# Kernel optimization log

Hardware: AMD Instinct MI355X
Metric: run time of the kernel (lower is better)

The kernel has to match this reference:

```python
import jax, jax.numpy as jnp
import numpy as np

DECAY = 0.99
EPS = 1e-05
LOSS_FACTOR = 0.1


def setup_inputs() -> dict:
    key = jax.random.key(0)
    k1, k2, k3, k4 = jax.random.split(key, 4)
    x = jax.random.normal(k1, (64, 256, 32, 32), dtype=jnp.float32)
    centroids = jax.random.normal(k2, (256, 1024), dtype=jnp.float32)
    cluster_size = jax.random.uniform(k3, (1024,), dtype=jnp.float32)
    centroids_avg = jax.random.normal(k4, (256, 1024), dtype=jnp.float32)
    return {"x": x, "centroids": centroids, "cluster_size": cluster_size,
            "centroids_avg": centroids_avg}


def _forward(x, centroids, cluster_size, centroids_avg):
    F, K = centroids.shape
    # torch: x_flat = x.transpose(-1, 1).contiguous().view(-1, n_features)
    xs = jnp.swapaxes(x, 1, -1)              # [B, W, H, C]
    flat_shape = xs.shape
    xf = xs.reshape(-1, F)                   # [N, F]
    dist = ((xf * xf).sum(1, keepdims=True)
            + (centroids * centroids).sum(0, keepdims=True)
            - 2.0 * (xf @ centroids))        # [N, K]
    ind = jnp.argmin(dist, axis=1)           # [N] nearest centroid
    # training-path EMA updates (one-hot matmuls expressed as segment sums)
    counts = jax.ops.segment_sum(jnp.ones(ind.shape, dtype=xf.dtype), ind,
                                 num_segments=K)              # [K]
    centroids_sum = jax.ops.segment_sum(xf, ind, num_segments=K).T  # [F, K]
    new_cs = DECAY * cluster_size + (1.0 - DECAY) * counts
    new_avg = DECAY * centroids_avg + (1.0 - DECAY) * centroids_sum
    n = new_cs.sum()
    cs_norm = (new_cs + EPS) / (n + K * EPS) * n
    new_centroids = new_avg / cs_norm[None, :]               # [F, K]
    # quantize with updated codebook (embedding lookup)
    xq = new_centroids.T[ind].reshape(flat_shape)            # [B, W, H, C]
    xq = jnp.swapaxes(xq, 1, -1)                             # [B, C, H, W]
    xq_st = x + jax.lax.stop_gradient(xq - x)                # straight-through
    return xq_st, xq


def reference(x, centroids, cluster_size, centroids_avg):
    out, _ = _forward(x, centroids, cluster_size, centroids_avg)
    return out
```

## Files before the change

### kernel.cpp

```cpp
#include <hip/hip_runtime.h>


#define DECAY 0.99f
#define EPSF 1e-5f
#define DELTA 0.05f

typedef _Float16 f16x8 __attribute__((ext_vector_type(8)));
typedef float f32x4 __attribute__((ext_vector_type(4)));

static __device__ __forceinline__ unsigned short h_bits(_Float16 h) {
  return __builtin_bit_cast(unsigned short, h);
}
static __device__ __forceinline__ float h_val(unsigned short u) {
  return (float)__builtin_bit_cast(_Float16, u);
}

__global__ void csq_kernel(const float* __restrict__ cent, float* __restrict__ csq) {
  int k0 = blockIdx.x * 64;
  int t = threadIdx.x;
  int kk = t & 63, cg = t >> 6;
  float s = 0.f;
  for (int c = cg; c < 256; c += 4) {
    float v = cent[(size_t)c * 1024 + k0 + kk];
    s += v * v;
  }
  __shared__ float red[4][64];
  red[cg][kk] = s;
  __syncthreads();
  if (t < 64) csq[k0 + t] = red[0][t] + red[1][t] + red[2][t] + red[3][t];
}

__global__ void centT_kernel(const float* __restrict__ cent, _Float16* __restrict__ ctp) {
  __shared__ float tl[32][33];
  int f0 = (blockIdx.x >> 5) * 32, k0 = (blockIdx.x & 31) * 32;
  int t = threadIdx.x;
#pragma unroll
  for (int i = 0; i < 4; ++i) {
    int fi = (t >> 5) + i * 8, ki = t & 31;
    tl[fi][ki] = cent[(size_t)(f0 + fi) * 1024 + k0 + ki];
  }
  __syncthreads();
#pragma unroll
  for (int i = 0; i < 4; ++i) {
    int ki = (t >> 5) + i * 8, fi = t & 31;
    int k = k0 + ki, f = f0 + fi;
    _Float16 h = (_Float16)tl[fi][ki];
    size_t idx = (size_t)(k >> 4) * 4096 + (size_t)(f >> 5) * 512 +
                 (size_t)(k & 15) * 32 + (size_t)((f >> 3) & 3) * 8 + (f & 7);
    ctp[idx] = h;
  }
}

__global__ void transpose_kernel(const float* __restrict__ x, _Float16* __restrict__ xh,
                                 _Float16* __restrict__ xl) {
  __shared__ float tile[64][65];
  int bid = blockIdx.x;
  int pt = bid & 15, ct = (bid >> 4) & 3, b = bid >> 6;
  int c0 = ct * 64, p0 = pt * 64;
  int t = threadIdx.x;
#pragma unroll
  for (int i = 0; i < 16; ++i) {
    int idx = t + i * 256;
    int ci = idx >> 6, pi = idx & 63;
    tile[ci][pi] = x[((size_t)(b * 256 + c0 + ci) << 10) + p0 + pi];
  }
  __syncthreads();
#pragma unroll
  for (int i = 0; i < 8; ++i) {
    int idx = t + i * 256;
    int pi = idx >> 5, cp = idx & 31;
    int p = p0 + pi;
    int r = ((p & 31) << 5) | (p >> 5);
    float v0 = tile[cp * 2][pi], v1 = tile[cp * 2 + 1][pi];
    _Float16 h0 = (_Float16)v0, h1 = (_Float16)v1;
    _Float16 l0 = (_Float16)(v0 - (float)h0), l1 = (_Float16)(v1 - (float)h1);
    unsigned int uh = (unsigned int)h_bits(h0) | ((unsigned int)h_bits(h1) << 16);
    unsigned int ul = (unsigned int)h_bits(l0) | ((unsigned int)h_bits(l1) << 16);
    size_t base = ((size_t)((b << 10) + r)) * 128 + ct * 32 + cp;
    ((unsigned int*)xh)[base] = uh;
    ((unsigned int*)xl)[base] = ul;
  }
}

__global__ __launch_bounds__(256, 3) void mfma_argmin_kernel(
    const _Float16* __restrict__ xh, const _Float16* __restrict__ ctp,
    const float* __restrict__ csq, int* __restrict__ ind,
    int* __restrict__ flaglist, unsigned int* __restrict__ flagcnt,
    unsigned int* __restrict__ counts) {
  __shared__ _Float16 Ah[64 * 256];
  __shared__ float csql[1024];
  __shared__ float red1[4][64], red2[4][64];
  __shared__ int redk[4][64];
  const int t = threadIdx.x;
  const int lane = t & 63, w = t >> 6;
  const int lr = lane & 15, lg = lane >> 4;
  const int n0 = blockIdx.x * 64;

#pragma unroll
  for (int i = 0; i < 4; ++i) csql[t + i * 256] = csq[t + i * 256];
#pragma unroll
  for (int i = 0; i < 8; ++i) {
    int idx = t + i * 256;
    int row = idx >> 5, c16 = (idx & 31) * 16;
    int sw = c16 ^ ((row & 7) << 4);
    *(f16x8*)((char*)Ah + row * 512 + sw) =
        *(const f16x8*)((const char*)xh + (size_t)(n0 + row) * 512 + c16);
  }
  __syncthreads();

  float b1[4][4], b2v[4][4];
  int bk[4][4];
#pragma unroll
  for (int rt = 0; rt < 4; ++rt)
#pragma unroll
    for (int rg = 0; rg < 4; ++rg) { b1[rt][rg] = 3.4e38f; b2v[rt][rg] = 3.4e38f; bk[rt][rg] = 0; }

  const int swz = (lr & 7) << 4;
  const int boff = (lr * 4 + lg) * 16;
#pragma unroll 1
  for (int ch = 0; ch < 4; ++ch) {
    const int ccb = w * 256 + ch * 64;
    const size_t cbase = (size_t)(ccb >> 4) * 8192 + boff;
    f32x4 acc[4][4];
#pragma unroll
    for (int ct = 0; ct < 4; ++ct)
#pragma unroll
      for (int rt = 0; rt < 4; ++rt) acc[ct][rt] = (f32x4){0.f, 0.f, 0.f, 0.f};

#pragma unroll 1
    for (int ks = 0; ks < 8; ++ks) {
      f16x8 bh[4], ah[4];
#pragma unroll
      for (int ct = 0; ct < 4; ++ct)
        bh[ct] = *(const f16x8*)((const char*)ctp + cbase + (size_t)ct * 8192 + ks * 1024);
#pragma unroll
      for (int rt = 0; rt < 4; ++rt)
        ah[rt] = *(const f16x8*)((const char*)Ah + (rt * 16 + lr) * 512 + ((ks * 64 + lg * 16) ^ swz));
#pragma unroll
      for (int ct = 0; ct < 4; ++ct)
#pragma unroll
        for (int rt = 0; rt < 4; ++rt)
          acc[ct][rt] = __builtin_amdgcn_mfma_f32_16x16x32_f16(ah[rt], bh[ct], acc[ct][rt], 0, 0, 0);
    }
#pragma unroll
    for (int ct = 0; ct < 4; ++ct) {
      const int col = ccb + ct * 16 + lr;
      const float cq = csql[col];
#pragma unroll
      for (int rt = 0; rt < 4; ++rt)
#pragma unroll
        for (int rg = 0; rg < 4; ++rg) {
          float d = cq - 2.f * acc[ct][rt][rg];
          if (d < b1[rt][rg]) {
            b2v[rt][rg] = b1[rt][rg];
            b1[rt][rg] = d;
            bk[rt][rg] = col;
          } else if (d < b2v[rt][rg]) {
            b2v[rt][rg] = d;
          }
        }
    }
  }

#pragma unroll
  for (int rt = 0; rt < 4; ++rt)
#pragma unroll
    for (int rg = 0; rg < 4; ++rg) {
      float v1 = b1[rt][rg], v2 = b2v[rt][rg];
      int kk = bk[rt][rg];
#pragma unroll
      for (int off = 8; off >= 1; off >>= 1) {
        float o1 = __shfl_xor(v1, off);
        int ok = __shfl_xor(kk, off);
        float o2 = __shfl_xor(v2, off);
        float nb2 = fminf(fmaxf(v1, o1), fminf(v2, o2));
        if (o1 < v1 || (o1 == v1 && ok < kk)) { v1 = o1; kk = ok; }
        v2 = nb2;
      }
      if (lr == 0) {
        int row = rt * 16 + lg * 4 + rg;
        red1[w][row] = v1;
        redk[w][row] = kk;
        red2[w][row] = v2;
      }
    }
  __syncthreads();
  if (t < 64) {
    float v1 = red1[0][t], v2 = red2[0][t];
    int kk = redk[0][t];
#pragma unroll
    for (int wi = 1; wi < 4; ++wi) {
      float o1 = red1[wi][t], o2 = red2[wi][t];
      int ok = redk[wi][t];
      float nb2 = fminf(fmaxf(v1, o1), fminf(v2, o2));
      if (o1 < v1 || (o1 == v1 && ok < kk)) { v1 = o1; kk = ok; }
      v2 = nb2;
    }
    ind[n0 + t] = kk;
    atomicAdd(&counts[kk], 1u);
    if (v2 - v1 < DELTA) {
      unsigned int p = atomicAdd(flagcnt, 1u);
      flaglist[p] = n0 + t;
    }
  }
}

__global__ __launch_bounds__(256) void fixup_kernel(
    const _Float16* __restrict__ xh, const _Float16* __restrict__ xl,
    const float* __restrict__ cent, const float* __restrict__ csq,
    const int* __restrict__ flaglist, const unsigned int* __restrict__ flagcnt,
    int* __restrict__ ind, unsigned int* __restrict__ counts) {
  const int t = threadIdx.x;
  const int nf = (int)*flagcnt;
  __shared__ float xrow[256];
  __shared__ float rv[256];
  __shared__ int rk[256];
  for (int ii = blockIdx.x; ii < nf; ii += gridDim.x) {
    __syncthreads();
    int row = flaglist[ii];
    xrow[t] = (float)xh[(size_t)row * 256 + t] + (float)xl[(size_t)row * 256 + t];
    __syncthreads();
    float a0 = 0.f, a1 = 0.f, a2 = 0.f, a3 = 0.f;
#pragma unroll 8
    for (int f = 0; f < 256; ++f) {
      float xs = xrow[f];
      const float* cr = cent + (size_t)f * 1024 + t;
      a0 += xs * cr[0];
      a1 += xs * cr[256];
      a2 += xs * cr[512];
      a3 += xs * cr[768];
    }
    float bd = csq[t] - 2.f * a0;
    int bkk = t;
    float d1 = csq[t + 256] - 2.f * a1;
    if (d1 < bd) { bd = d1; bkk = t + 256; }
    float d2 = csq[t + 512] - 2.f * a2;
    if (d2 < bd) { bd = d2; bkk = t + 512; }
    float d3 = csq[t + 768] - 2.f * a3;
    if (d3 < bd) { bd = d3; bkk = t + 768; }
    rv[t] = bd;
    rk[t] = bkk;
    __syncthreads();
    for (int off = 128; off >= 1; off >>= 1) {
      if (t < off) {
        float ov = rv[t + off];
        int ok = rk[t + off];
        if (ov < rv[t] || (ov == rv[t] && ok < rk[t])) { rv[t] = ov; rk[t] = ok; }
      }
      __syncthreads();
    }
    if (t == 0) {
      int newk = rk[0];
      int oldk = ind[row];
      if (newk != oldk) {
        ind[row] = newk;
        atomicAdd(&counts[oldk], 0xFFFFFFFFu);
        atomicAdd(&counts[newk], 1u);
      }
    }
  }
}

__global__ __launch_bounds__(64) void csnorm_scan_kernel(
    const float* __restrict__ cs, const unsigned int* __restrict__ counts,
    float* __restrict__ icn, unsigned int* __restrict__ offsets,
    unsigned int* __restrict__ cursor) {
  const int t = threadIdx.x;
  unsigned int cl[16];
  float csl[16];
  unsigned int s = 0;
  float css = 0.f;
#pragma unroll
  for (int j = 0; j < 16; ++j) {
    cl[j] = counts[t * 16 + j];
    s += cl[j];
    csl[j] = cs[t * 16 + j];
    css += csl[j];
  }
  unsigned int incl = s;
#pragma unroll
  for (int off = 1; off < 64; off <<= 1) {
    unsigned int v = __shfl_up(incl, off);
    if (t >= off) incl += v;
  }
  unsigned int run = incl - s;
  float tot = css;
#pragma unroll
  for (int off = 32; off >= 1; off >>= 1) tot += __shfl_xor(tot, off);
  const float n = DECAY * tot + (1.f - DECAY) * 65536.f;
#pragma unroll
  for (int j = 0; j < 16; ++j) {
    int k = t * 16 + j;
    offsets[k] = run;
    cursor[k] = run;
    float ncs = DECAY * csl[j] + (1.f - DECAY) * (float)cl[j];
    float csn = (ncs + EPSF) / (n + 1024.f * EPSF) * n;
    icn[k] = 1.f / csn;
    run += cl[j];
  }
  if (t == 63) offsets[1024] = run;
}

__global__ void scatter_kernel(const int* __restrict__ ind, unsigned int* __restrict__ cursor,
                               int* __restrict__ rowlist) {
  int n = blockIdx.x * 256 + threadIdx.x;
  int k = ind[n];
  unsigned int pos = atomicAdd(&cursor[k], 1u);
  rowlist[pos] = n;
}

__global__ __launch_bounds__(256) void sumflush_kernel(
    const _Float16* __restrict__ xh, const int* __restrict__ rowlist,
    const int* __restrict__ ind, float* __restrict__ sums) {
  __shared__ int rl[64];
  __shared__ int kl[64];
  const int t = threadIdx.x;
  const int sub = t >> 6, lane = t & 63;
  const int p0 = blockIdx.x * 64;
  if (t < 64) {
    int r = rowlist[p0 + t];
    rl[t] = r;
    kl[t] = ind[r];
  }
  __syncthreads();
  float a0 = 0.f, a1 = 0.f, a2 = 0.f, a3 = 0.f;
  int curk = kl[sub * 16];
#pragma unroll
  for (int i = 0; i < 16; ++i) {
    int p = sub * 16 + i;
    int k = kl[p];
    if (k != curk) {
      float* dst = &sums[(size_t)curk * 256 + lane * 4];
      atomicAdd(&dst[0], a0);
      atomicAdd(&dst[1], a1);
      atomicAdd(&dst[2], a2);
      atomicAdd(&dst[3], a3);
      a0 = a1 = a2 = a3 = 0.f;
      curk = k;
    }
    int r = rl[p];
    uint2 vh = *(const uint2*)&((const unsigned int*)xh)[(size_t)r * 128 + lane * 2];
    a0 += h_val((unsigned short)(vh.x & 0xFFFF));
    a1 += h_val((unsigned short)(vh.x >> 16));
    a2 += h_val((unsigned short)(vh.y & 0xFFFF));
    a3 += h_val((unsigned short)(vh.y >> 16));
  }
  float* dst = &sums[(size_t)curk * 256 + lane * 4];
  atomicAdd(&dst[0], a0);
  atomicAdd(&dst[1], a1);
  atomicAdd(&dst[2], a2);
  atomicAdd(&dst[3], a3);
}

__global__ __launch_bounds__(256) void newcentT_kernel(
    const float* __restrict__ sums, const float* __restrict__ avg,
    const float* __restrict__ icn, float* __restrict__ nc) {
  __shared__ float tl[32][33];
  const int t = threadIdx.x;
  const int k0 = (blockIdx.x & 31) * 32, f0 = (blockIdx.x >> 5) * 32;
#pragma unroll
  for (int i = 0; i < 4; ++i) {
    int ki = (t >> 5) + i * 8, fi = t & 31;
    tl[ki][fi] = sums[(size_t)(k0 + ki) * 256 + f0 + fi];
  }
  __syncthreads();
#pragma unroll
  for (int i = 0; i < 4; ++i) {
    int fi = (t >> 5) + i * 8, ki = t & 31;
    size_t idx = (size_t)(f0 + fi) * 1024 + k0 + ki;
    nc[idx] = (DECAY * avg[idx] + (1.f - DECAY) * tl[ki][fi]) * icn[k0 + ki];
  }
}

__global__ void gather_kernel(const float* __restrict__ nc, const int* __restrict__ ind,
                              float* __restrict__ out) {
  __shared__ int ip[1024];
  int b = blockIdx.x >> 3;
  int cg = (blockIdx.x & 7) * 32;
  int t = threadIdx.x;
#pragma unroll
  for (int j = 0; j < 4; ++j) {
    int p = t + j * 256;
    int r = ((p & 31) << 5) | (p >> 5);
    ip[p] = ind[(b << 10) + r];
  }
  __syncthreads();
  for (int c = cg; c < cg + 32; ++c) {
    const float* row = nc + (size_t)c * 1024;
#pragma unroll
    for (int j = 0; j < 4; ++j) {
      int p = t + j * 256;
      out[((size_t)(b * 256 + c) << 10) + p] = row[ip[p]];
    }
  }
}

extern "C" void kernel_launch(void* const* d_in, const int* in_sizes, int n_in,
                              void* d_out, int out_size, void* d_ws, size_t ws_size,
                              hipStream_t stream) {
  const float* x = (const float*)d_in[0];
  const float* cent = (const float*)d_in[1];
  const float* cs = (const float*)d_in[2];
  const float* avg = (const float*)d_in[3];
  float* out = (float*)d_out;

  char* ws = (char*)d_ws;
  _Float16* xh = (_Float16*)ws;
  _Float16* xl = (_Float16*)(ws + 33554432);
  _Float16* ctp = (_Float16*)(ws + 67108864);
  float* nc = (float*)(ws + 67108864);
  unsigned int* counts = (unsigned int*)(ws + 68157440);
  unsigned int* flagcnt = (unsigned int*)(ws + 68161536);
  float* csq = (float*)(ws + 68165632);
  float* icn = (float*)(ws + 68169728);
  unsigned int* offsets = (unsigned int*)(ws + 68173824);
  unsigned int* cursor = (unsigned int*)(ws + 68182016);
  int* ind = (int*)(ws + 68186112);
  int* flaglist = (int*)(ws + 68448256);
  int* rowlist = (int*)(ws + 68448256);
  float* sums = (float*)(ws + 68710400);

  hipMemsetAsync(counts, 0, 8192, stream);
  hipMemsetAsync(sums, 0, 1048576, stream);

  csq_kernel<<<16, 256, 0, stream>>>(cent, csq);
  centT_kernel<<<256, 256, 0, stream>>>(cent, ctp);
  transpose_kernel<<<4096, 256, 0, stream>>>(x, xh, xl);
  mfma_argmin_kernel<<<1024, 256, 0, stream>>>(xh, ctp, csq, ind, flaglist, flagcnt, counts);
  fixup_kernel<<<128, 256, 0, stream>>>(xh, xl, cent, csq, flaglist, flagcnt, ind, counts);
  csnorm_scan_kernel<<<1, 64, 0, stream>>>(cs, counts, icn, offsets, cursor);
  scatter_kernel<<<256, 256, 0, stream>>>(ind, cursor, rowlist);
  sumflush_kernel<<<1024, 256, 0, stream>>>(xh, rowlist, ind, sums);
  newcentT_kernel<<<256, 256, 0, stream>>>(sums, avg, icn, nc);
  gather_kernel<<<512, 256, 0, stream>>>(nc, ind, out);
}
```

Before: 290.4 us.

## Double-buffer centroid tiles into LDS via async global_load_lds in argmin MFMA loop

```diff
diff --git a/kernel.cpp b/kernel.cpp
--- a/kernel.cpp
+++ b/kernel.cpp
@@ -82,12 +82,13 @@
   }
 }
 
-__global__ __launch_bounds__(256, 3) void mfma_argmin_kernel(
+__global__ __launch_bounds__(256, 2) void mfma_argmin_kernel(
     const _Float16* __restrict__ xh, const _Float16* __restrict__ ctp,
     const float* __restrict__ csq, int* __restrict__ ind,
     int* __restrict__ flaglist, unsigned int* __restrict__ flagcnt,
     unsigned int* __restrict__ counts) {
   __shared__ _Float16 Ah[64 * 256];
+  __shared__ _Float16 Bst[4 * 2 * 4 * 512];
   __shared__ float csql[1024];
   __shared__ float red1[4][64], red2[4][64];
   __shared__ int redk[4][64];
@@ -116,32 +117,87 @@
     for (int rg = 0; rg < 4; ++rg) { b1[rt][rg] = 3.4e38f; b2v[rt][rg] = 3.4e38f; bk[rt][rg] = 0; }
 
   const int swz = (lr & 7) << 4;
-  const int boff = (lr * 4 + lg) * 16;
+  const int boffh = (lr * 4 + lg) * 8;
+  const size_t lgo = (size_t)lane * 16;
+  _Float16* bw = &Bst[w * 4096];
+
+#define DMA4(CHB, KS, P)                                                              \
+  do {                                                                                \
+    const char* g_ = (const char*)ctp + (CHB) + (size_t)(KS) * 1024 + lgo;            \
+    _Float16* l_ = bw + (P) * 2048;                                                   \
+    __builtin_amdgcn_global_load_lds(                                                 \
+        (const __attribute__((address_space(1))) unsigned int*)(g_),                  \
+        (__attribute__((address_space(3))) unsigned int*)(l_), 16, 0, 0);             \
+    __builtin_amdgcn_global_load_lds(                                                 \
+        (const __attribute__((address_space(1))) unsigned int*)(g_ + 8192),           \
+        (__attribute__((address_space(3))) unsigned int*)(l_ + 512), 16, 0, 0);       \
+    __builtin_amdgcn_global_load_lds(                                                 \
+        (const __attribute__((address_space(1))) unsigned int*)(g_ + 16384),          \
+        (__attribute__((address_space(3))) unsigned int*)(l_ + 1024), 16, 0, 0);      \
+    __builtin_amdgcn_global_load_lds(                                                 \
+        (const __attribute__((address_space(1))) unsigned int*)(g_ + 24576),          \
+        (__attribute__((address_space(3))) unsigned int*)(l_ + 1536), 16, 0, 0);      \
+  } while (0)
+
+#define KSHALF(KS, P, WN)                                                             \
+  do {                                                                                \
+    asm volatile("s_waitcnt vmcnt(" WN ")" ::: "memory");                             \
+    __builtin_amdgcn_sched_barrier(0);                                                \
+    const _Float16* bp_ = bw + (P) * 2048 + boffh;                                    \
+    f16x8 q0 = *(const f16x8*)(bp_);                                                  \
+    f16x8 q1 = *(const f16x8*)(bp_ + 512);                                            \
+    f16x8 q2 = *(const f16x8*)(bp_ + 1024);                                           \
+    f16x8 q3 = *(const f16x8*)(bp_ + 1536);                                           \
+    const char* ap_ = (const char*)Ah + lr * 512 + (((KS) * 64 + lg * 16) ^ swz);     \
+    f16x8 p0 = *(const f16x8*)(ap_);                                                  \
+    f16x8 p1 = *(const f16x8*)(ap_ + 8192);                                           \
+    f16x8 p2 = *(const f16x8*)(ap_ + 16384);                                          \
+    f16x8 p3 = *(const f16x8*)(ap_ + 24576);                                          \
+    acc[0][0] = __builtin_amdgcn_mfma_f32_16x16x32_f16(p0, q0, acc[0][0], 0, 0, 0);   \
+    acc[0][1] = __builtin_amdgcn_mfma_f32_16x16x32_f16(p1, q0, acc[0][1], 0, 0, 0);   \
+    acc[0][2] = __builtin_amdgcn_mfma_f32_16x16x32_f16(p2, q0, acc[0][2], 0, 0, 0);   \
+    acc[0][3] = __builtin_amdgcn_mfma_f32_16x16x32_f16(p3, q0, acc[0][3], 0, 0, 0);   \
+    acc[1][0] = __builtin_amdgcn_mfma_f32_16x16x32_f16(p0, q1, acc[1][0], 0, 0, 0);   \
+    acc[1][1] = __builtin_amdgcn_mfma_f32_16x16x32_f16(p1, q1, acc[1][1], 0, 0, 0);   \
+    acc[1][2] = __builtin_amdgcn_mfma_f32_16x16x32_f16(p2, q1, acc[1][2], 0, 0, 0);   \
+    acc[1][3] = __builtin_amdgcn_mfma_f32_16x16x32_f16(p3, q1, acc[1][3], 0, 0, 0);   \
+    acc[2][0] = __builtin_amdgcn_mfma_f32_16x16x32_f16(p0, q2, acc[2][0], 0, 0, 0);   \
+    acc[2][1] = __builtin_amdgcn_mfma_f32_16x16x32_f16(p1, q2, acc[2][1], 0, 0, 0);   \
+    acc[2][2] = __builtin_amdgcn_mfma_f32_16x16x32_f16(p2, q2, acc[2][2], 0, 0, 0);   \
+    acc[2][3] = __builtin_amdgcn_mfma_f32_16x16x32_f16(p3, q2, acc[2][3], 0, 0, 0);   \
+    acc[3][0] = __builtin_amdgcn_mfma_f32_16x16x32_f16(p0, q3, acc[3][0], 0, 0, 0);   \
+    acc[3][1] = __builtin_amdgcn_mfma_f32_16x16x32_f16(p1, q3, acc[3][1], 0, 0, 0);   \
+    acc[3][2] = __builtin_amdgcn_mfma_f32_16x16x32_f16(p2, q3, acc[3][2], 0, 0, 0);   \
+    acc[3][3] = __builtin_amdgcn_mfma_f32_16x16x32_f16(p3, q3, acc[3][3], 0, 0, 0);   \
+  } while (0)
+
+  size_t chb = (size_t)w * 131072;
+  DMA4(chb, 0, 0);
+  DMA4(chb, 1, 1);
 #pragma unroll 1
   for (int ch = 0; ch < 4; ++ch) {
     const int ccb = w * 256 + ch * 64;
-    const size_t cbase = (size_t)(ccb >> 4) * 8192 + boff;
     f32x4 acc[4][4];
 #pragma unroll
     for (int ct = 0; ct < 4; ++ct)
 #pragma unroll
       for (int rt = 0; rt < 4; ++rt) acc[ct][rt] = (f32x4){0.f, 0.f, 0.f, 0.f};
 
-#pragma unroll 1
-    for (int ks = 0; ks < 8; ++ks) {
-      f16x8 bh[4], ah[4];
-#pragma unroll
-      for (int ct = 0; ct < 4; ++ct)
-        bh[ct] = *(const f16x8*)((const char*)ctp + cbase + (size_t)ct * 8192 + ks * 1024);
-#pragma unroll
-      for (int rt = 0; rt < 4; ++rt)
-        ah[rt] = *(const f16x8*)((const char*)Ah + (rt * 16 + lr) * 512 + ((ks * 64 + lg * 16) ^ swz));
-#pragma unroll
-      for (int ct = 0; ct < 4; ++ct)
-#pragma unroll
-        for (int rt = 0; rt < 4; ++rt)
-          acc[ct][rt] = __builtin_amdgcn_mfma_f32_16x16x32_f16(ah[rt], bh[ct], acc[ct][rt], 0, 0, 0);
-    }
+    KSHALF(0, 0, "4");  DMA4(chb, 2, 0);
+    KSHALF(1, 1, "4");  DMA4(chb, 3, 1);
+    KSHALF(2, 0, "4");  DMA4(chb, 4, 0);
+    KSHALF(3, 1, "4");  DMA4(chb, 5, 1);
+    KSHALF(4, 0, "4");  DMA4(chb, 6, 0);
+    KSHALF(5, 1, "4");  DMA4(chb, 7, 1);
+    KSHALF(6, 0, "4");
+    if (ch < 3) {
+      DMA4(chb + 32768, 0, 0);
+      KSHALF(7, 1, "4");
+      DMA4(chb + 32768, 1, 1);
+    } else {
+      KSHALF(7, 1, "0");
+    }
+
 #pragma unroll
     for (int ct = 0; ct < 4; ++ct) {
       const int col = ccb + ct * 16 + lr;
@@ -160,7 +216,10 @@
           }
         }
     }
-  }
+    chb += 32768;
+  }
+#undef DMA4
+#undef KSHALF
 
 #pragma unroll
   for (int rt = 0; rt < 4; ++rt)
@@ -411,23 +470,22 @@
   float* nc = (float*)(ws + 67108864);
   unsigned int* counts = (unsigned int*)(ws + 68157440);
   unsigned int* flagcnt = (unsigned int*)(ws + 68161536);
-  float* csq = (float*)(ws + 68165632);
-  float* icn = (float*)(ws + 68169728);
-  unsigned int* offsets = (unsigned int*)(ws + 68173824);
-  unsigned int* cursor = (unsigned int*)(ws + 68182016);
-  int* ind = (int*)(ws + 68186112);
-  int* flaglist = (int*)(ws + 68448256);
-  int* rowlist = (int*)(ws + 68448256);
-  float* sums = (float*)(ws + 68710400);
-
-  hipMemsetAsync(counts, 0, 8192, stream);
-  hipMemsetAsync(sums, 0, 1048576, stream);
-
-  csq_kernel<<<16, 256, 0, stream>>>(cent, csq);
+  float* sums = (float*)(ws + 68165632);
+  float* csqv = (float*)(ws + 69214208);
+  float* icn = (float*)(ws + 69218304);
+  unsigned int* offsets = (unsigned int*)(ws + 69222400);
+  unsigned int* cursor = (unsigned int*)(ws + 69230592);
+  int* ind = (int*)(ws + 69234688);
+  int* flaglist = (int*)(ws + 69496832);
+  int* rowlist = (int*)(ws + 69496832);
+
+  hipMemsetAsync(counts, 0, 1056768, stream);
+
+  csq_kernel<<<16, 256, 0, stream>>>(cent, csqv);
   centT_kernel<<<256, 256, 0, stream>>>(cent, ctp);
   transpose_kernel<<<4096, 256, 0, stream>>>(x, xh, xl);
-  mfma_argmin_kernel<<<1024, 256, 0, stream>>>(xh, ctp, csq, ind, flaglist, flagcnt, counts);
-  fixup_kernel<<<128, 256, 0, stream>>>(xh, xl, cent, csq, flaglist, flagcnt, ind, counts);
+  mfma_argmin_kernel<<<1024, 256, 0, stream>>>(xh, ctp, csqv, ind, flaglist, flagcnt, counts);
+  fixup_kernel<<<128, 256, 0, stream>>>(xh, xl, cent, csqv, flaglist, flagcnt, ind, counts);
   csnorm_scan_kernel<<<1, 64, 0, stream>>>(cs, counts, icn, offsets, cursor);
   scatter_kernel<<<256, 256, 0, stream>>>(ind, cursor, rowlist);
   sumflush_kernel<<<1024, 256, 0, stream>>>(xh, rowlist, ind, sums);
```

New measurement: 277.9 us. -4.3%, faster.
